# Performance work log

Hardware: AMD Instinct MI355X
Metric: run time of the kernel (lower is better)

## Reference

```python
import jax, jax.numpy as jnp
import numpy as np


def _gcn_layer(x, row, col, W, b):
    # x: [N, d_in]; row/col: [E'] (with self loops already appended)
    N = x.shape[0]
    deg = jax.ops.segment_sum(jnp.ones_like(row, dtype=x.dtype), row, num_segments=N)
    deg_inv_sqrt = deg ** -0.5  # self loops guarantee deg >= 1
    norm = deg_inv_sqrt[row] * deg_inv_sqrt[col]  # [E']
    msg = norm[:, None] * x[row]                  # gather + normalize
    aggr = jax.ops.segment_sum(msg, col, num_segments=N)  # scatter-add
    return aggr @ W + b


def reference(x, edge_index, W1, b1, W2, b2):
    N = x.shape[0]
    loops = jnp.arange(N, dtype=edge_index.dtype)
    row = jnp.concatenate([edge_index[0], loops])
    col = jnp.concatenate([edge_index[1], loops])
    h = jax.nn.relu(_gcn_layer(x, row, col, W1, b1))
    # F.dropout(training=self.training) is identity in eval mode
    out = _gcn_layer(h, row, col, W2, b2)
    return jax.nn.log_softmax(out, axis=1)


def setup_inputs() -> dict:
    key = jax.random.key(0)
    k1, k2, k3, k4 = jax.random.split(key, 4)
    N, E, F_IN, F_HID, F_OUT = 100000, 1200000, 64, 64, 16
    x = jax.random.normal(k1, (N, F_IN), dtype=jnp.float32)
    edge_index = jax.random.randint(k2, (2, E), 0, N, dtype=jnp.int64)
    W1 = jax.random.normal(k3, (F_IN, F_HID), dtype=jnp.float32) / np.sqrt(F_IN)
    b1 = jnp.zeros((F_HID,), dtype=jnp.float32)
    W2 = jax.random.normal(k4, (F_HID, F_OUT), dtype=jnp.float32) / np.sqrt(F_HID)
    b2 = jnp.zeros((F_OUT,), dtype=jnp.float32)
    return {"x": x, "edge_index": edge_index, "W1": W1, "b1": b1, "W2": W2, "b2": b2}
```

## Files before the change

### kernel.cpp

```cpp
#include <hip/hip_runtime.h>
#include <hip/hip_bf16.h>

typedef __attribute__((ext_vector_type(8))) _Float16 hfrag;
typedef __attribute__((ext_vector_type(4))) float ffrag;
typedef __attribute__((ext_vector_type(4))) _Float16 h4v;

#define BSH 8
#define LBS 256
#define CAP_SH 14
#define CAP (1 << CAP_SH)
#define NF 256
#define CONV_BLKS 384

__device__ __forceinline__ float b2f_(unsigned short u) {
    return __uint_as_float(((unsigned)u) << 16);
}
__device__ __forceinline__ unsigned short f2b_(float v) {
    __hip_bfloat16 h = __float2bfloat16(v);
    return *reinterpret_cast<unsigned short*>(&h);
}
__device__ __forceinline__ unsigned short f2h_(float v) {
    _Float16 h = (_Float16)v;
    return __builtin_bit_cast(unsigned short, h);
}
__device__ __forceinline__ float h2f_(unsigned short u) {
    _Float16 h = __builtin_bit_cast(_Float16, u);
    return (float)h;
}

__device__ __forceinline__ float loadF(const void* p, long long i, int isF32) {
    if (isF32) return ((const float*)p)[i];
    return b2f_(((const unsigned short*)p)[i]);
}

__device__ __forceinline__ float4 loadF4(const void* p, long long base, int i4, int isF32) {
    if (isF32) {
        return ((const float4*)((const float*)p + base))[i4];
    } else {
        ushort4 u = ((const ushort4*)((const unsigned short*)p + base))[i4];
        return make_float4(b2f_(u.x), b2f_(u.y), b2f_(u.z), b2f_(u.w));
    }
}

__device__ __forceinline__ void get_edge(const int* ei, int i64, int e, int E, int& s, int& d) {
    if (i64) { s = ei[2 * (long long)e]; d = ei[2 * (long long)E + 2 * (long long)e]; }
    else     { s = ei[e];                d = ei[(long long)E + e]; }
}

struct E4 { int s[4]; int d[4]; };
__device__ __forceinline__ E4 load4(const int* __restrict__ ei, int i64, int e0, int E) {
    E4 r;
    if (i64) {
        const int4* ps = (const int4*)(ei + 2 * (long long)e0);
        const int4* pd = (const int4*)(ei + 2 * (long long)E + 2 * (long long)e0);
        int4 a = ps[0], b = ps[1];
        int4 c = pd[0], d = pd[1];
        r.s[0] = a.x; r.s[1] = a.z; r.s[2] = b.x; r.s[3] = b.z;
        r.d[0] = c.x; r.d[1] = c.z; r.d[2] = d.x; r.d[3] = d.z;
    } else {
        int4 a = *(const int4*)(ei + e0);
        int4 c = *(const int4*)(ei + (long long)E + e0);
        r.s[0] = a.x; r.s[1] = a.y; r.s[2] = a.z; r.s[3] = a.w;
        r.d[0] = c.x; r.d[1] = c.y; r.d[2] = c.z; r.d[3] = c.w;
    }
    return r;
}

__device__ __forceinline__ void wave_scan_excl(int* a, int nEl, int lane) {
    int run = 0;
    for (int base = 0; base < nEl; base += 64) {
        int i = base + lane;
        int orig = (i < nEl) ? a[i] : 0;
        int v = orig;
#pragma unroll
        for (int off = 1; off < 64; off <<= 1) {
            int u = __shfl_up(v, off);
            if (lane >= off) v += u;
        }
        if (i < nEl) a[i] = v - orig + run;
        run += __shfl(v, 63);
    }
}

__global__ __launch_bounds__(256) void k_hist(const void* __restrict__ x,
                                              const int* __restrict__ ei,
                                              const void* __restrict__ W1, const void* __restrict__ b1,
                                              const void* __restrict__ W2, const void* __restrict__ b2,
                                              int E, int N, int nbk,
                                              int* __restrict__ flags, float* __restrict__ Wbuf,
                                              int* __restrict__ cnt_d, int* __restrict__ cnt_s,
                                              unsigned short* __restrict__ xh) {
    __shared__ int hd[512], hs[512];
    __shared__ int s_sane, s_zero;
    int tid = threadIdx.x;
    if (tid == 0) { s_sane = 0; s_zero = 0; }
    __syncthreads();
    const unsigned short* xu = (const unsigned short*)x;
    if (blockIdx.x == NF) {
        int sane = 0;
        for (int k = tid; k < 4096; k += 256) {
            float v = b2f_(xu[2 * k]);
            float a = fabsf(v);
            if (v == 0.0f || (a >= 9.3e-10f && a <= 1.1e9f)) sane++;
        }
        if (sane) atomicAdd(&s_sane, sane);
        int zero = 0;
        for (int k = tid; k < 1024; k += 256) if (ei[2 * k + 1] == 0) zero++;
        if (zero) atomicAdd(&s_zero, zero);
        __syncthreads();
        int f = (s_sane < 3000) ? 1 : 0;
        if (tid == 0) { flags[0] = f; flags[1] = (s_zero > 512) ? 1 : 0; }
        for (int i = tid; i < 4096; i += 256) Wbuf[i] = loadF(W1, i, f);
        if (tid < 64) Wbuf[4096 + tid] = loadF(b1, tid, f);
        for (int i = tid; i < 1024; i += 256) Wbuf[4160 + i] = loadF(W2, i, f);
        if (tid < 16) Wbuf[5184 + tid] = loadF(b2, tid, f);
        return;
    }
    if (blockIdx.x > NF) {
        int cb = blockIdx.x - NF - 1;
        int sane = 0;
        for (int k = tid; k < 4096; k += 256) {
            float v = b2f_(xu[2 * k]);
            float a = fabsf(v);
            if (v == 0.0f || (a >= 9.3e-10f && a <= 1.1e9f)) sane++;
        }
        if (sane) atomicAdd(&s_sane, sane);
        __syncthreads();
        int f = (s_sane < 3000) ? 1 : 0;
        int n4 = N * 16;
        int ctid = cb * 256 + tid;
        int stride = CONV_BLKS * 256 * 2;
        for (int i0 = ctid * 2; i0 < n4; i0 += stride) {
            float4 v0 = loadF4(x, 0, i0, f);
            float4 v1 = (i0 + 1 < n4) ? loadF4(x, 0, i0 + 1, f) : make_float4(0, 0, 0, 0);
            ushort4 o0, o1;
            o0.x = f2h_(v0.x); o0.y = f2h_(v0.y); o0.z = f2h_(v0.z); o0.w = f2h_(v0.w);
            o1.x = f2h_(v1.x); o1.y = f2h_(v1.y); o1.z = f2h_(v1.z); o1.w = f2h_(v1.w);
            ((ushort4*)xh)[i0] = o0;
            if (i0 + 1 < n4) ((ushort4*)xh)[i0 + 1] = o1;
        }
        return;
    }
    int zero = 0;
    for (int k = tid; k < 1024; k += 256) if (ei[2 * k + 1] == 0) zero++;
    if (zero) atomicAdd(&s_zero, zero);
    for (int i = tid; i < 512; i += 256) { hd[i] = 0; hs[i] = 0; }
    __syncthreads();
    int i64 = (s_zero > 512) ? 1 : 0;
    int fb = blockIdx.x;
    int ctid = fb * 256 + tid;
    int stride = NF * 256 * 8;
    for (int e0 = ctid * 8; e0 + 8 <= E; e0 += stride) {
        E4 a = load4(ei, i64, e0, E);
        E4 b = load4(ei, i64, e0 + 4, E);
#pragma unroll
        for (int u = 0; u < 4; ++u) {
            atomicAdd(&hd[a.d[u] >> BSH], 1);
            atomicAdd(&hs[a.s[u] >> BSH], 1);
            atomicAdd(&hd[b.d[u] >> BSH], 1);
            atomicAdd(&hs[b.s[u] >> BSH], 1);
        }
    }
    if (fb == 0 && tid == 0) {
        for (int e = E & ~7; e < E; ++e) {
            int s, d;
            get_edge(ei, i64, e, E, s, d);
            atomicAdd(&hd[d >> BSH], 1);
            atomicAdd(&hs[s >> BSH], 1);
        }
    }
    __syncthreads();
    for (int b = tid; b < nbk; b += 256) {
        cnt_d[b * NF + fb] = hd[b];
        cnt_s[b * NF + fb] = hs[b];
    }
}

__global__ __launch_bounds__(256) void k_fill(const int* __restrict__ ei,
                                              int E, int nbk,
                                              const int* __restrict__ cnt_d,
                                              const int* __restrict__ cnt_s,
                                              int* __restrict__ td, int* __restrict__ ts,
                                              int* __restrict__ pdst,
                                              unsigned char* __restrict__ psrc) {
    __shared__ int bd[512], bs[512];
    __shared__ int s_zero;
    int tid = threadIdx.x;
    if (tid == 0) s_zero = 0;
    __syncthreads();
    int zero = 0;
    for (int k = tid; k < 1024; k += 256) if (ei[2 * k + 1] == 0) zero++;
    if (zero) atomicAdd(&s_zero, zero);
    int fb = blockIdx.x;
    for (int b = tid; b < nbk; b += 256) {
        int pre_d = 0, tot_d = 0, pre_s = 0, tot_s = 0;
        const int* rd = cnt_d + b * NF;
        const int* rs = cnt_s + b * NF;
        for (int j = 0; j < NF; j += 4) {
            int4 vd = *(const int4*)(rd + j);
            int4 vs = *(const int4*)(rs + j);
            tot_d += vd.x + vd.y + vd.z + vd.w;
            tot_s += vs.x + vs.y + vs.z + vs.w;
            if (j + 0 < fb) { pre_d += vd.x; pre_s += vs.x; }
            if (j + 1 < fb) { pre_d += vd.y; pre_s += vs.y; }
            if (j + 2 < fb) { pre_d += vd.z; pre_s += vs.z; }
            if (j + 3 < fb) { pre_d += vd.w; pre_s += vs.w; }
        }
        bd[b] = (b << CAP_SH) + pre_d;
        bs[b] = (b << CAP_SH) + pre_s;
        if (fb == 0) { td[b] = (b << CAP_SH) + tot_d; ts[b] = (b << CAP_SH) + tot_s; }
    }
    __syncthreads();
    int i64 = (s_zero > 512) ? 1 : 0;
    int ctid = fb * 256 + tid;
    int stride = NF * 256 * 8;
    for (int e0 = ctid * 8; e0 + 8 <= E; e0 += stride) {
        E4 a = load4(ei, i64, e0, E);
        E4 b = load4(ei, i64, e0 + 4, E);
#pragma unroll
        for (int u = 0; u < 4; ++u) {
            int db = a.d[u] >> BSH, sb = a.s[u] >> BSH;
            int p = atomicAdd(&bd[db], 1);
            if (p < ((db + 1) << CAP_SH)) pdst[p] = (a.s[u] << BSH) | (a.d[u] & (LBS - 1));
            int q = atomicAdd(&bs[sb], 1);
            if (q < ((sb + 1) << CAP_SH)) psrc[q] = (unsigned char)(a.s[u] & (LBS - 1));
            db = b.d[u] >> BSH; sb = b.s[u] >> BSH;
            p = atomicAdd(&bd[db], 1);
            if (p < ((db + 1) << CAP_SH)) pdst[p] = (b.s[u] << BSH) | (b.d[u] & (LBS - 1));
            q = atomicAdd(&bs[sb], 1);
            if (q < ((sb + 1) << CAP_SH)) psrc[q] = (unsigned char)(b.s[u] & (LBS - 1));
        }
    }
    if (fb == 0 && tid == 0) {
        for (int e = E & ~7; e < E; ++e) {
            int s, d;
            get_edge(ei, i64, e, E, s, d);
            int db = d >> BSH, sb = s >> BSH;
            int p = atomicAdd(&bd[db], 1);
            if (p < ((db + 1) << CAP_SH)) pdst[p] = (s << BSH) | (d & (LBS - 1));
            int q = atomicAdd(&bs[sb], 1);
            if (q < ((sb + 1) << CAP_SH)) psrc[q] = (unsigned char)(s & (LBS - 1));
        }
    }
}

__global__ __launch_bounds__(256) void k_deg(const unsigned char* __restrict__ psrc,
                                             const int* __restrict__ ts,
                                             float* __restrict__ dis, int N) {
    __shared__ int h[LBS];
    int b = blockIdx.x, tid = threadIdx.x;
    if (tid < LBS) h[tid] = 0;
    __syncthreads();
    int beg = b << CAP_SH;
    int end = min(ts[b], (b + 1) << CAP_SH);
    int cnt = end - beg;
    int nv = cnt & ~3;
    for (int off = 4 * tid; off < nv; off += 1024) {
        uchar4 v = *(const uchar4*)(psrc + beg + off);
        atomicAdd(&h[v.x], 1); atomicAdd(&h[v.y], 1);
        atomicAdd(&h[v.z], 1); atomicAdd(&h[v.w], 1);
    }
    if (tid < cnt - nv) atomicAdd(&h[psrc[beg + nv + tid]], 1);
    __syncthreads();
    if (tid < LBS) {
        int node = b * LBS + tid;
        if (node < N) dis[node] = rsqrtf((float)h[tid] + 1.0f);
    }
}

__global__ __launch_bounds__(256) void k_csr(const int* __restrict__ pdst,
                                             const int* __restrict__ td,
                                             const float* __restrict__ dis,
                                             int2* __restrict__ row_se,
                                             int2* __restrict__ pke, int N) {
    __shared__ int h[LBS], lb[LBS], cur[LBS];
    int b = blockIdx.x, tid = threadIdx.x;
    if (tid < LBS) h[tid] = 0;
    __syncthreads();
    int beg = b << CAP_SH;
    int end = min(td[b], (b + 1) << CAP_SH);
    for (int p = beg + tid; p < end; p += 256) atomicAdd(&h[pdst[p] & (LBS - 1)], 1);
    __syncthreads();
    if (tid < LBS) lb[tid] = h[tid];
    __syncthreads();
    if (tid < 64) wave_scan_excl(lb, LBS, tid);
    __syncthreads();
    if (tid < LBS) {
        cur[tid] = lb[tid];
        int node = b * LBS + tid;
        if (node < N) row_se[node] = make_int2(beg + lb[tid], beg + lb[tid] + h[tid]);
    }
    __syncthreads();
    for (int p = beg + tid; p < end; p += 256) {
        int e = pdst[p];
        int src = e >> BSH, ld = e & (LBS - 1);
        int r = atomicAdd(&cur[ld], 1);
        pke[beg + r] = make_int2(src, __float_as_int(dis[src]));
    }
}

__global__ __launch_bounds__(256) void k_agg(const unsigned short* __restrict__ xh,
                                             const float* __restrict__ dis,
                                             const int2* __restrict__ row_se,
                                             const int2* __restrict__ pke,
                                             unsigned short* __restrict__ aggb, int N) {
    int tid = threadIdx.x;
    int lane = tid & 63;
    int g = lane >> 4, i4 = lane & 15;
    int n = blockIdx.x * 16 + (tid >> 6) * 4 + g;
    if (n >= N) return;
    float dd = dis[n];
    int2 se = row_se[n];
    int beg = se.x, end = se.y;
    int cnt = end - beg;
    h4v xv = *(const h4v*)(xh + (long long)n * 64 + i4 * 4);
    float w = dd * dd;
    float4 A[4];
    A[0].x = w * (float)xv[0]; A[0].y = w * (float)xv[1];
    A[0].z = w * (float)xv[2]; A[0].w = w * (float)xv[3];
#pragma unroll
    for (int u = 1; u < 4; ++u) A[u] = make_float4(0.f, 0.f, 0.f, 0.f);
    int T = (cnt + 3) >> 2;
    int p = beg;
    int2 e[4];
#pragma unroll
    for (int u = 0; u < 4; ++u) e[u] = pke[p + u];
    for (int t = 0; t < T; ++t) {
        h4v hv[4];
#pragma unroll
        for (int u = 0; u < 4; ++u) {
            unsigned ex = min((unsigned)e[u].x, (unsigned)(N - 1));
            hv[u] = *(const h4v*)(xh + (long long)ex * 64 + i4 * 4);
        }
        float nv[4];
#pragma unroll
        for (int u = 0; u < 4; ++u) nv[u] = (p + u < end) ? dd * __int_as_float(e[u].y) : 0.f;
#pragma unroll
        for (int u = 0; u < 4; ++u) e[u] = pke[p + 4 + u];
        p += 4;
#pragma unroll
        for (int u = 0; u < 4; ++u) {
            A[u].x += nv[u] * (float)hv[u][0];
            A[u].y += nv[u] * (float)hv[u][1];
            A[u].z += nv[u] * (float)hv[u][2];
            A[u].w += nv[u] * (float)hv[u][3];
        }
    }
    float4 s;
    s.x = A[0].x + A[1].x + A[2].x + A[3].x;
    s.y = A[0].y + A[1].y + A[2].y + A[3].y;
    s.z = A[0].z + A[1].z + A[2].z + A[3].z;
    s.w = A[0].w + A[1].w + A[2].w + A[3].w;
    ushort4 o;
    o.x = f2h_(s.x); o.y = f2h_(s.y); o.z = f2h_(s.z); o.w = f2h_(s.w);
    *(ushort4*)(aggb + (size_t)n * 64 + i4 * 4) = o;
}

__global__ __launch_bounds__(256) void k_dense(const unsigned short* __restrict__ aggb,
                                               const float* __restrict__ Wbuf,
                                               unsigned short* __restrict__ t2b, int N) {
    __shared__ __align__(16) unsigned short Hs[4][16 * 72];
    int tid = threadIdx.x;
    int lane = tid & 63;
    int w = tid >> 6;
    int m = lane & 15, q = lane >> 4;
    int n0 = blockIdx.x * 64 + w * 16;
    if (n0 >= N) return;

    hfrag Bw1[2][4];
#pragma unroll
    for (int kt = 0; kt < 2; ++kt)
#pragma unroll
        for (int nt = 0; nt < 4; ++nt)
#pragma unroll
            for (int j = 0; j < 8; ++j)
                Bw1[kt][nt][j] = (_Float16)Wbuf[(kt * 32 + q * 8 + j) * 64 + nt * 16 + m];
    hfrag Bw2[2];
#pragma unroll
    for (int kt = 0; kt < 2; ++kt)
#pragma unroll
        for (int j = 0; j < 8; ++j)
            Bw2[kt][j] = (_Float16)Wbuf[4160 + (kt * 32 + q * 8 + j) * 16 + m];
    float b1n[4];
#pragma unroll
    for (int nt = 0; nt < 4; ++nt) b1n[nt] = Wbuf[4096 + nt * 16 + m];

    const unsigned short* arow = aggb + (size_t)(n0 + m) * 64 + q * 8;
    hfrag A0 = *(const hfrag*)(arow);
    hfrag A1 = *(const hfrag*)(arow + 32);

    ffrag acc[4];
#pragma unroll
    for (int nt = 0; nt < 4; ++nt) {
        ffrag z = {0.f, 0.f, 0.f, 0.f};
        z = __builtin_amdgcn_mfma_f32_16x16x32_f16(A0, Bw1[0][nt], z, 0, 0, 0);
        z = __builtin_amdgcn_mfma_f32_16x16x32_f16(A1, Bw1[1][nt], z, 0, 0, 0);
        acc[nt] = z;
    }
    unsigned short* hs = &Hs[w][0];
#pragma unroll
    for (int nt = 0; nt < 4; ++nt)
#pragma unroll
        for (int r = 0; r < 4; ++r) {
            float hv = fmaxf(acc[nt][r] + b1n[nt], 0.0f);
            hs[(q * 4 + r) * 72 + nt * 16 + m] = f2h_(hv);
        }
    const unsigned short* hrow = hs + m * 72 + q * 8;
    hfrag H0 = *(const hfrag*)(hrow);
    hfrag H1 = *(const hfrag*)(hrow + 32);
    ffrag t2 = {0.f, 0.f, 0.f, 0.f};
    t2 = __builtin_amdgcn_mfma_f32_16x16x32_f16(H0, Bw2[0], t2, 0, 0, 0);
    t2 = __builtin_amdgcn_mfma_f32_16x16x32_f16(H1, Bw2[1], t2, 0, 0, 0);
#pragma unroll
    for (int r = 0; r < 4; ++r)
        t2b[(size_t)(n0 + q * 4 + r) * 16 + m] = f2h_(t2[r]);
}

__global__ __launch_bounds__(256) void k_l2(const unsigned short* __restrict__ t2b,
                                            const int* __restrict__ flags,
                                            const float* __restrict__ dis,
                                            const int2* __restrict__ row_se,
                                            const int2* __restrict__ pke,
                                            const float* __restrict__ Wbuf,
                                            void* __restrict__ out, int N) {
    int isF32 = flags[0];
    int tid = threadIdx.x, lane = tid & 63;
    int g = lane >> 4, i = lane & 15;
    int n = blockIdx.x * 16 + (tid >> 6) * 4 + g;
    if (n >= N) return;
    float dd = dis[n];
    int2 se = row_se[n];
    int beg = se.x, end = se.y;
    int cnt = end - beg;
    float A[4];
    A[0] = dd * dd * h2f_(t2b[(size_t)n * 16 + i]);
    A[1] = 0.f; A[2] = 0.f; A[3] = 0.f;
    int T = (cnt + 3) >> 2;
    int p = beg;
    int2 e[4];
#pragma unroll
    for (int u = 0; u < 4; ++u) e[u] = pke[p + u];
    for (int t = 0; t < T; ++t) {
        float r[4];
#pragma unroll
        for (int u = 0; u < 4; ++u) {
            unsigned ex = min((unsigned)e[u].x, (unsigned)(N - 1));
            r[u] = h2f_(t2b[(size_t)ex * 16 + i]);
        }
        float nv[4];
#pragma unroll
        for (int u = 0; u < 4; ++u) nv[u] = (p + u < end) ? dd * __int_as_float(e[u].y) : 0.f;
#pragma unroll
        for (int u = 0; u < 4; ++u) e[u] = pke[p + 4 + u];
        p += 4;
#pragma unroll
        for (int u = 0; u < 4; ++u) A[u] += nv[u] * r[u];
    }
    float a0 = A[0] + A[1] + A[2] + A[3];
    float v = a0 + Wbuf[5184 + i];
    float mx = v;
#pragma unroll
    for (int off = 8; off; off >>= 1) mx = fmaxf(mx, __shfl_xor(mx, off, 16));
    float ex = __expf(v - mx);
    float ss = ex;
#pragma unroll
    for (int off = 8; off; off >>= 1) ss += __shfl_xor(ss, off, 16);
    float r = v - mx - logf(ss);
    size_t oi = (size_t)n * 16 + i;
    if (isF32) ((float*)out)[oi] = r;
    else       ((unsigned short*)out)[oi] = f2b_(r);
}

extern "C" void kernel_launch(void* const* d_in, const int* in_sizes, int n_in,
                              void* d_out, int out_size, void* d_ws, size_t ws_size,
                              hipStream_t stream) {
    const void* x  = d_in[0];
    const int*  ei = (const int*)d_in[1];
    const void* W1 = d_in[2];
    const void* b1 = d_in[3];
    const void* W2 = d_in[4];
    const void* b2 = d_in[5];

    const int N = in_sizes[0] / 64;
    const int E = in_sizes[1] / 2;
    const int nbk = (N + LBS - 1) >> BSH;

    char* p = (char*)d_ws;
#define CARVE(ty, name, bytes) ty name = (ty)p; p += (((size_t)(bytes)) + 63) & ~(size_t)63;
    CARVE(int*,   flags,     16)
    CARVE(float*, Wbuf,      5200 * 4)
    CARVE(float*, dis,       (size_t)N * 4)
    CARVE(int2*,  row_se,    (size_t)N * 8)
    CARVE(int*,   cnt_d,     (size_t)nbk * NF * 4)
    CARVE(int*,   cnt_s,     (size_t)nbk * NF * 4)
    CARVE(int*,   td,        (size_t)nbk * 4)
    CARVE(int*,   ts,        (size_t)nbk * 4)
    CARVE(int*,   pdst,      ((size_t)nbk << CAP_SH) * 4)
    CARVE(unsigned char*, psrc, ((size_t)nbk << CAP_SH))
    CARVE(int2*,  pke,       (((size_t)nbk << CAP_SH) + 64) * 8)
    CARVE(unsigned short*, xh,   (size_t)N * 64 * 2)
    CARVE(unsigned short*, aggb, (size_t)N * 64 * 2)
    CARVE(unsigned short*, t2b,  (size_t)N * 16 * 2)
#undef CARVE

    k_hist<<<NF + 1 + CONV_BLKS, 256, 0, stream>>>(x, ei, W1, b1, W2, b2, E, N, nbk,
                                                   flags, Wbuf, cnt_d, cnt_s, xh);
    k_fill<<<NF, 256, 0, stream>>>(ei, E, nbk, cnt_d, cnt_s, td, ts, pdst, psrc);
    k_deg<<<nbk, 256, 0, stream>>>(psrc, ts, dis, N);
    k_csr<<<nbk, 256, 0, stream>>>(pdst, td, dis, row_se, pke, N);
    k_agg<<<(N + 15) / 16, 256, 0, stream>>>(xh, dis, row_se, pke, aggb, N);
    k_dense<<<(N + 63) / 64, 256, 0, stream>>>(aggb, Wbuf, t2b, N);
    k_l2<<<(N + 15) / 16, 256, 0, stream>>>(t2b, flags, dis, row_se, pke, Wbuf, d_out, N);
}
```

Before: 223.6 us.

## Merge histogram and fill into single per-block local bucketing pass

Replaces the two-pass global counting sort (histogram kernel, then a fill kernel that computes global prefix offsets) with one kernel. Each of 1024 blocks owns a contiguous edge chunk, scans its own bucket histogram and scatters edges into its private region, writing per-block bucket offsets. The degree and CSR kernels then walk the 1024 per-block segments per bucket. This removes a kernel launch and a second read of the edge list. In exchange the downstream kernels perform serial per-thread loops over many short segments with scattered reads.

After: 205.0 us. 8.3% less time.

```diff
diff --git a/kernel.cpp b/kernel.cpp
--- a/kernel.cpp
+++ b/kernel.cpp
@@ -9,7 +9,8 @@
 #define LBS 256
 #define CAP_SH 14
 #define CAP (1 << CAP_SH)
-#define NF 256
+#define NF 1024
+#define OPAD 520
 #define CONV_BLKS 384
 
 __device__ __forceinline__ float b2f_(unsigned short u) {
@@ -82,15 +83,17 @@
     }
 }
 
-__global__ __launch_bounds__(256) void k_hist(const void* __restrict__ x,
-                                              const int* __restrict__ ei,
-                                              const void* __restrict__ W1, const void* __restrict__ b1,
-                                              const void* __restrict__ W2, const void* __restrict__ b2,
-                                              int E, int N, int nbk,
-                                              int* __restrict__ flags, float* __restrict__ Wbuf,
-                                              int* __restrict__ cnt_d, int* __restrict__ cnt_s,
-                                              unsigned short* __restrict__ xh) {
-    __shared__ int hd[512], hs[512];
+__global__ __launch_bounds__(256) void k_stage(const void* __restrict__ x,
+                                               const int* __restrict__ ei,
+                                               const void* __restrict__ W1, const void* __restrict__ b1,
+                                               const void* __restrict__ W2, const void* __restrict__ b2,
+                                               int E, int N, int nbk, int EPB,
+                                               int* __restrict__ flags, float* __restrict__ Wbuf,
+                                               int* __restrict__ off_d, int* __restrict__ off_s,
+                                               int* __restrict__ pdst,
+                                               unsigned char* __restrict__ psrc,
+                                               unsigned short* __restrict__ xh) {
+    __shared__ int hd[512], hs[512], cd[512], cs[512];
     __shared__ int s_sane, s_zero;
     int tid = threadIdx.x;
     if (tid == 0) { s_sane = 0; s_zero = 0; }
@@ -148,154 +151,114 @@
     __syncthreads();
     int i64 = (s_zero > 512) ? 1 : 0;
     int fb = blockIdx.x;
-    int ctid = fb * 256 + tid;
-    int stride = NF * 256 * 8;
-    for (int e0 = ctid * 8; e0 + 8 <= E; e0 += stride) {
+    int elo = fb * EPB;
+    int ehi = min(elo + EPB, E);
+    if (elo >= E) {
+        for (int b = tid; b <= nbk; b += 256) {
+            off_d[fb * OPAD + b] = E; off_s[fb * OPAD + b] = E;
+        }
+        return;
+    }
+    int ecnt = ehi - elo;
+    for (int e0 = elo + tid * 4; e0 + 4 <= ehi; e0 += 1024) {
         E4 a = load4(ei, i64, e0, E);
-        E4 b = load4(ei, i64, e0 + 4, E);
 #pragma unroll
         for (int u = 0; u < 4; ++u) {
             atomicAdd(&hd[a.d[u] >> BSH], 1);
             atomicAdd(&hs[a.s[u] >> BSH], 1);
-            atomicAdd(&hd[b.d[u] >> BSH], 1);
-            atomicAdd(&hs[b.s[u] >> BSH], 1);
-        }
-    }
-    if (fb == 0 && tid == 0) {
-        for (int e = E & ~7; e < E; ++e) {
-            int s, d;
-            get_edge(ei, i64, e, E, s, d);
-            atomicAdd(&hd[d >> BSH], 1);
-            atomicAdd(&hs[s >> BSH], 1);
-        }
-    }
+        }
+    }
+    int rem = ecnt & 3, ebase = elo + (ecnt & ~3);
+    if (tid < rem) {
+        int s, d;
+        get_edge(ei, i64, ebase + tid, E, s, d);
+        atomicAdd(&hd[d >> BSH], 1);
+        atomicAdd(&hs[s >> BSH], 1);
+    }
+    __syncthreads();
+    if (tid < 64)       wave_scan_excl(hd, nbk, tid);
+    else if (tid < 128) wave_scan_excl(hs, nbk, tid - 64);
     __syncthreads();
     for (int b = tid; b < nbk; b += 256) {
-        cnt_d[b * NF + fb] = hd[b];
-        cnt_s[b * NF + fb] = hs[b];
-    }
-}
-
-__global__ __launch_bounds__(256) void k_fill(const int* __restrict__ ei,
-                                              int E, int nbk,
-                                              const int* __restrict__ cnt_d,
-                                              const int* __restrict__ cnt_s,
-                                              int* __restrict__ td, int* __restrict__ ts,
-                                              int* __restrict__ pdst,
-                                              unsigned char* __restrict__ psrc) {
-    __shared__ int bd[512], bs[512];
-    __shared__ int s_zero;
-    int tid = threadIdx.x;
-    if (tid == 0) s_zero = 0;
-    __syncthreads();
-    int zero = 0;
-    for (int k = tid; k < 1024; k += 256) if (ei[2 * k + 1] == 0) zero++;
-    if (zero) atomicAdd(&s_zero, zero);
-    int fb = blockIdx.x;
-    for (int b = tid; b < nbk; b += 256) {
-        int pre_d = 0, tot_d = 0, pre_s = 0, tot_s = 0;
-        const int* rd = cnt_d + b * NF;
-        const int* rs = cnt_s + b * NF;
-        for (int j = 0; j < NF; j += 4) {
-            int4 vd = *(const int4*)(rd + j);
-            int4 vs = *(const int4*)(rs + j);
-            tot_d += vd.x + vd.y + vd.z + vd.w;
-            tot_s += vs.x + vs.y + vs.z + vs.w;
-            if (j + 0 < fb) { pre_d += vd.x; pre_s += vs.x; }
-            if (j + 1 < fb) { pre_d += vd.y; pre_s += vs.y; }
-            if (j + 2 < fb) { pre_d += vd.z; pre_s += vs.z; }
-            if (j + 3 < fb) { pre_d += vd.w; pre_s += vs.w; }
-        }
-        bd[b] = (b << CAP_SH) + pre_d;
-        bs[b] = (b << CAP_SH) + pre_s;
-        if (fb == 0) { td[b] = (b << CAP_SH) + tot_d; ts[b] = (b << CAP_SH) + tot_s; }
-    }
-    __syncthreads();
-    int i64 = (s_zero > 512) ? 1 : 0;
-    int ctid = fb * 256 + tid;
-    int stride = NF * 256 * 8;
-    for (int e0 = ctid * 8; e0 + 8 <= E; e0 += stride) {
+        int od = elo + hd[b], os = elo + hs[b];
+        off_d[fb * OPAD + b] = od; cd[b] = od;
+        off_s[fb * OPAD + b] = os; cs[b] = os;
+    }
+    if (tid == 0) { off_d[fb * OPAD + nbk] = elo + ecnt; off_s[fb * OPAD + nbk] = elo + ecnt; }
+    __syncthreads();
+    for (int e0 = elo + tid * 4; e0 + 4 <= ehi; e0 += 1024) {
         E4 a = load4(ei, i64, e0, E);
-        E4 b = load4(ei, i64, e0 + 4, E);
 #pragma unroll
         for (int u = 0; u < 4; ++u) {
-            int db = a.d[u] >> BSH, sb = a.s[u] >> BSH;
-            int p = atomicAdd(&bd[db], 1);
-            if (p < ((db + 1) << CAP_SH)) pdst[p] = (a.s[u] << BSH) | (a.d[u] & (LBS - 1));
-            int q = atomicAdd(&bs[sb], 1);
-            if (q < ((sb + 1) << CAP_SH)) psrc[q] = (unsigned char)(a.s[u] & (LBS - 1));
-            db = b.d[u] >> BSH; sb = b.s[u] >> BSH;
-            p = atomicAdd(&bd[db], 1);
-            if (p < ((db + 1) << CAP_SH)) pdst[p] = (b.s[u] << BSH) | (b.d[u] & (LBS - 1));
-            q = atomicAdd(&bs[sb], 1);
-            if (q < ((sb + 1) << CAP_SH)) psrc[q] = (unsigned char)(b.s[u] & (LBS - 1));
-        }
-    }
-    if (fb == 0 && tid == 0) {
-        for (int e = E & ~7; e < E; ++e) {
-            int s, d;
-            get_edge(ei, i64, e, E, s, d);
-            int db = d >> BSH, sb = s >> BSH;
-            int p = atomicAdd(&bd[db], 1);
-            if (p < ((db + 1) << CAP_SH)) pdst[p] = (s << BSH) | (d & (LBS - 1));
-            int q = atomicAdd(&bs[sb], 1);
-            if (q < ((sb + 1) << CAP_SH)) psrc[q] = (unsigned char)(s & (LBS - 1));
-        }
+            int p = atomicAdd(&cd[a.d[u] >> BSH], 1);
+            pdst[p] = (a.s[u] << BSH) | (a.d[u] & (LBS - 1));
+            int q = atomicAdd(&cs[a.s[u] >> BSH], 1);
+            psrc[q] = (unsigned char)(a.s[u] & (LBS - 1));
+        }
+    }
+    if (tid < rem) {
+        int s, d;
+        get_edge(ei, i64, ebase + tid, E, s, d);
+        int p = atomicAdd(&cd[d >> BSH], 1);
+        pdst[p] = (s << BSH) | (d & (LBS - 1));
+        int q = atomicAdd(&cs[s >> BSH], 1);
+        psrc[q] = (unsigned char)(s & (LBS - 1));
     }
 }
 
 __global__ __launch_bounds__(256) void k_deg(const unsigned char* __restrict__ psrc,
-                                             const int* __restrict__ ts,
-                                             float* __restrict__ dis, int N) {
+                                             const int* __restrict__ off_s,
+                                             float* __restrict__ dis, int N, int nbk) {
     __shared__ int h[LBS];
     int b = blockIdx.x, tid = threadIdx.x;
-    if (tid < LBS) h[tid] = 0;
-    __syncthreads();
-    int beg = b << CAP_SH;
-    int end = min(ts[b], (b + 1) << CAP_SH);
-    int cnt = end - beg;
-    int nv = cnt & ~3;
-    for (int off = 4 * tid; off < nv; off += 1024) {
-        uchar4 v = *(const uchar4*)(psrc + beg + off);
-        atomicAdd(&h[v.x], 1); atomicAdd(&h[v.y], 1);
-        atomicAdd(&h[v.z], 1); atomicAdd(&h[v.w], 1);
-    }
-    if (tid < cnt - nv) atomicAdd(&h[psrc[beg + nv + tid]], 1);
-    __syncthreads();
-    if (tid < LBS) {
-        int node = b * LBS + tid;
-        if (node < N) dis[node] = rsqrtf((float)h[tid] + 1.0f);
-    }
+    h[tid] = 0;
+    __syncthreads();
+    for (int fb = tid; fb < NF; fb += 256) {
+        int o0 = off_s[fb * OPAD + b];
+        int o1 = off_s[fb * OPAD + b + 1];
+        for (int p = o0; p < o1; ++p) atomicAdd(&h[psrc[p]], 1);
+    }
+    __syncthreads();
+    int node = b * LBS + tid;
+    if (node < N) dis[node] = rsqrtf((float)h[tid] + 1.0f);
 }
 
 __global__ __launch_bounds__(256) void k_csr(const int* __restrict__ pdst,
-                                             const int* __restrict__ td,
+                                             const int* __restrict__ off_d,
                                              const float* __restrict__ dis,
                                              int2* __restrict__ row_se,
-                                             int2* __restrict__ pke, int N) {
+                                             int2* __restrict__ pke, int N, int nbk) {
     __shared__ int h[LBS], lb[LBS], cur[LBS];
     int b = blockIdx.x, tid = threadIdx.x;
-    if (tid < LBS) h[tid] = 0;
+    h[tid] = 0;
+    __syncthreads();
+    for (int fb = tid; fb < NF; fb += 256) {
+        int o0 = off_d[fb * OPAD + b];
+        int o1 = off_d[fb * OPAD + b + 1];
+        for (int p = o0; p < o1; ++p) atomicAdd(&h[pdst[p] & (LBS - 1)], 1);
+    }
+    __syncthreads();
+    lb[tid] = h[tid];
+    __syncthreads();
+    if (tid < 64) wave_scan_excl(lb, LBS, tid);
     __syncthreads();
     int beg = b << CAP_SH;
-    int end = min(td[b], (b + 1) << CAP_SH);
-    for (int p = beg + tid; p < end; p += 256) atomicAdd(&h[pdst[p] & (LBS - 1)], 1);
-    __syncthreads();
-    if (tid < LBS) lb[tid] = h[tid];
-    __syncthreads();
-    if (tid < 64) wave_scan_excl(lb, LBS, tid);
-    __syncthreads();
-    if (tid < LBS) {
-        cur[tid] = lb[tid];
-        int node = b * LBS + tid;
-        if (node < N) row_se[node] = make_int2(beg + lb[tid], beg + lb[tid] + h[tid]);
-    }
-    __syncthreads();
-    for (int p = beg + tid; p < end; p += 256) {
-        int e = pdst[p];
-        int src = e >> BSH, ld = e & (LBS - 1);
-        int r = atomicAdd(&cur[ld], 1);
-        pke[beg + r] = make_int2(src, __float_as_int(dis[src]));
+    cur[tid] = lb[tid];
+    int node = b * LBS + tid;
+    if (node < N) {
+        int s0 = min(lb[tid], CAP), s1 = min(lb[tid] + h[tid], CAP);
+        row_se[node] = make_int2(beg + s0, beg + s1);
+    }
+    __syncthreads();
+    for (int fb = tid; fb < NF; fb += 256) {
+        int o0 = off_d[fb * OPAD + b];
+        int o1 = off_d[fb * OPAD + b + 1];
+        for (int p = o0; p < o1; ++p) {
+            int e = pdst[p];
+            int src = e >> BSH, ld = e & (LBS - 1);
+            int r = atomicAdd(&cur[ld], 1);
+            if (r < CAP) pke[beg + r] = make_int2(src, __float_as_int(dis[src]));
+        }
     }
 }
 
@@ -484,6 +447,7 @@
     const int N = in_sizes[0] / 64;
     const int E = in_sizes[1] / 2;
     const int nbk = (N + LBS - 1) >> BSH;
+    const int EPB = (((E + NF - 1) / NF) + 7) & ~7;
 
     char* p = (char*)d_ws;
 #define CARVE(ty, name, bytes) ty name = (ty)p; p += (((size_t)(bytes)) + 63) & ~(size_t)63;
@@ -491,23 +455,22 @@
     CARVE(float*, Wbuf,      5200 * 4)
     CARVE(float*, dis,       (size_t)N * 4)
     CARVE(int2*,  row_se,    (size_t)N * 8)
-    CARVE(int*,   cnt_d,     (size_t)nbk * NF * 4)
-    CARVE(int*,   cnt_s,     (size_t)nbk * NF * 4)
-    CARVE(int*,   td,        (size_t)nbk * 4)
-    CARVE(int*,   ts,        (size_t)nbk * 4)
-    CARVE(int*,   pdst,      ((size_t)nbk << CAP_SH) * 4)
-    CARVE(unsigned char*, psrc, ((size_t)nbk << CAP_SH))
+    CARVE(int*,   off_d,     (size_t)NF * OPAD * 4)
+    CARVE(int*,   off_s,     (size_t)NF * OPAD * 4)
+    CARVE(int*,   pdst,      (size_t)NF * EPB * 4)
+    CARVE(unsigned char*, psrc, (size_t)NF * EPB)
     CARVE(int2*,  pke,       (((size_t)nbk << CAP_SH) + 64) * 8)
     CARVE(unsigned short*, xh,   (size_t)N * 64 * 2)
     CARVE(unsigned short*, aggb, (size_t)N * 64 * 2)
     CARVE(unsigned short*, t2b,  (size_t)N * 16 * 2)
 #undef CARVE
 
-    k_hist<<<NF + 1 + CONV_BLKS, 256, 0, stream>>>(x, ei, W1, b1, W2, b2, E, N, nbk,
-                                                   flags, Wbuf, cnt_d, cnt_s, xh);
-    k_fill<<<NF, 256, 0, stream>>>(ei, E, nbk, cnt_d, cnt_s, td, ts, pdst, psrc);
-    k_deg<<<nbk, 256, 0, stream>>>(psrc, ts, dis, N);
-    k_csr<<<nbk, 256, 0, stream>>>(pdst, td, dis, row_se, pke, N);
+    k_stage<<<NF + 1 + CONV_BLKS, 256, 0, stream>>>(x, ei, W1, b1, W2, b2,
+                                                    E, N, nbk, EPB,
+                                                    flags, Wbuf, off_d, off_s,
+                                                    pdst, psrc, xh);
+    k_deg<<<nbk, 256, 0, stream>>>(psrc, off_s, dis, N, nbk);
+    k_csr<<<nbk, 256, 0, stream>>>(pdst, off_d, dis, row_se, pke, N, nbk);
     k_agg<<<(N + 15) / 16, 256, 0, stream>>>(xh, dis, row_se, pke, aggb, N);
     k_dense<<<(N + 63) / 64, 256, 0, stream>>>(aggb, Wbuf, t2b, N);
     k_l2<<<(N + 15) / 16, 256, 0, stream>>>(t2b, flags, dis, row_se, pke, Wbuf, d_out, N);
```
